# Optimization experiments

Hardware: AMD Instinct MI355X
Metric: run time of the kernel (lower is better)

## Reference

```python
import jax, jax.numpy as jnp
import numpy as np

IN_CH = 128
OUT_CH = 32
HEADS = 4
N_NODES = 50000
N_EDGES = 500000
NEG_SLOPE = 0.01  # torch leaky_relu default


def setup_inputs() -> dict:
    key = jax.random.key(0)
    ks = jax.random.split(key, 8)
    E, D, H, C = N_EDGES, IN_CH, HEADS, OUT_CH
    receivers = jax.random.normal(ks[0], (E, D), dtype=jnp.float32)
    senders = jax.random.normal(ks[1], (E, D), dtype=jnp.float32)
    edge_attribute = jax.random.normal(ks[2], (E, D), dtype=jnp.float32)
    sender_idx = jax.random.randint(ks[3], (E,), 0, N_NODES)
    receiver_idx = jax.random.randint(ks[4], (E,), 0, N_NODES)
    # bias-free linear weights, stored as [in, heads*out] so y = x @ W
    scale = 1.0 / np.sqrt(D)
    W_src = jax.random.normal(ks[5], (D, H * C), dtype=jnp.float32) * scale
    W_tgt = jax.random.normal(ks[6], (D, H * C), dtype=jnp.float32) * scale
    W_edge = jax.random.normal(ks[7], (D, H * C), dtype=jnp.float32) * scale
    # xavier_normal_ on shape (1, H, C): std = sqrt(2/(H + C)) per torch fan calc on last two dims
    attn = jax.random.normal(jax.random.fold_in(key, 99), (1, H, C), dtype=jnp.float32) * np.sqrt(2.0 / (H + C))
    return {
        "receivers": receivers,
        "senders": senders,
        "edge_attribute": edge_attribute,
        "sender_idx": sender_idx,
        "receiver_idx": receiver_idx,
        "W_src": W_src,
        "W_tgt": W_tgt,
        "W_edge": W_edge,
        "attn": attn,
    }


def reference(receivers, senders, edge_attribute, sender_idx, receiver_idx, W_src, W_tgt, W_edge, attn):
    E = receivers.shape[0]
    H, C = HEADS, OUT_CH
    t = (receivers @ W_tgt).reshape(E, H, C)   # target projection of receiver feats
    s = (senders @ W_src).reshape(E, H, C)
    e = (edge_attribute @ W_edge).reshape(E, H, C)
    z = (jax.nn.leaky_relu(s + t + e, NEG_SLOPE) * attn).sum(-1)  # [E, H]
    # segment softmax over edges grouped by sender_idx
    zmax = jax.ops.segment_max(z, sender_idx, num_segments=N_NODES)  # [N, H]
    ez = jnp.exp(z - zmax[sender_idx])
    denom = jax.ops.segment_sum(ez, sender_idx, num_segments=N_NODES)
    a = ez / denom[sender_idx]                 # [E, H]
    m = t * a[..., None]                        # [E, H, C]
    aggr_m = jax.ops.segment_sum(m, receiver_idx, num_segments=N_NODES)  # [N, H, C]
    return aggr_m.mean(axis=1), m.mean(axis=1)  # ([N, C], [E, C])
```

## Files before the change

kernel.cpp:

```cpp
#include <hip/hip_runtime.h>
#include <hip/hip_bf16.h>

#define E_EDGES 500000
#define NN 50000

typedef unsigned short u16;
typedef __attribute__((ext_vector_type(8))) short s16x8;
typedef __attribute__((ext_vector_type(4))) float f32x4;

#define BAR() __builtin_amdgcn_s_barrier()
#define SCHED0() __builtin_amdgcn_sched_barrier(0)
#define WAITLGKM0() asm volatile("s_waitcnt lgkmcnt(0)" ::: "memory")

__device__ __forceinline__ short f2bf(float f) {
    unsigned u = __builtin_bit_cast(unsigned, f);
    u += 0x7fffu + ((u >> 16) & 1u);
    return (short)(u >> 16);
}

__device__ __forceinline__ float lrelu(float x) { return x > 0.0f ? x : 0.01f * x; }

__device__ __forceinline__ s16x8 cvt8(float4 lo, float4 hi) {
    union { s16x8 v; __hip_bfloat162 h[4]; } u;
    u.h[0] = __float22bfloat162_rn(make_float2(lo.x, lo.y));
    u.h[1] = __float22bfloat162_rn(make_float2(lo.z, lo.w));
    u.h[2] = __float22bfloat162_rn(make_float2(hi.x, hi.y));
    u.h[3] = __float22bfloat162_rn(make_float2(hi.z, hi.w));
    return u.v;
}

__global__ void kprep(const float* __restrict__ Wsrc, const float* __restrict__ Wtgt,
                      const float* __restrict__ Wedge, u16* __restrict__ WT) {
    int i = blockIdx.x * 256 + threadIdx.x;
    if (i >= 3 * 16384) return;
    int g = i >> 14, nk = i & 16383, n = nk >> 7, k = nk & 127;
    const float* W = (g == 0) ? Wsrc : (g == 1) ? Wtgt : Wedge;
    WT[i] = (u16)f2bf(W[k * 128 + n]);
}

__global__ __launch_bounds__(256, 2) void k1(
    const float* __restrict__ recv, const float* __restrict__ send,
    const float* __restrict__ eattr, const int* __restrict__ sidx,
    const u16* __restrict__ WT, const float* __restrict__ attn,
    float* __restrict__ ez, float* __restrict__ denom)
{
    __shared__ u16 ldsA[64][136];
    __shared__ float smEz[64][4];
    const int tid = threadIdx.x;
    const int lane = tid & 63, wv = tid >> 6;
    const int l15 = lane & 15, lg = (lane >> 4) & 3;
    const int b = blockIdx.x;

    const float* Xg[3] = {send, eattr, recv};
    const int bgoff[3] = {0, 2 * 16384, 1 * 16384};

    s16x8 bfr[3][4][2];
#pragma unroll
    for (int g = 0; g < 3; ++g)
#pragma unroll
        for (int kk = 0; kk < 4; ++kk)
#pragma unroll
            for (int nn = 0; nn < 2; ++nn)
                bfr[g][kk][nn] = *(const s16x8*)(WT + bgoff[g] +
                    ((wv * 2 + nn) * 16 + l15) * 128 + kk * 32 + lg * 8);

    const float av0 = attn[(wv * 2 + 0) * 16 + l15];
    const float av1 = attn[(wv * 2 + 1) * 16 + l15];

    f32x4 acc[4][2];
    float4 ra[4][2];

    auto issueA = [&](const float* X, int tileRow) {
#pragma unroll
        for (int q = 0; q < 4; ++q) {
            int idx = tid + 256 * q;
            int row = idx >> 4, gcol = (idx & 15) * 8;
            int ge = min(tileRow + row, E_EDGES - 1);
            const float* p = X + (size_t)ge * 128 + gcol;
            ra[q][0] = *(const float4*)p;
            ra[q][1] = *(const float4*)(p + 4);
        }
    };

    auto commitA = [&]() {
#pragma unroll
        for (int q = 0; q < 4; ++q) {
            int idx = tid + 256 * q;
            *(s16x8*)&ldsA[idx >> 4][(idx & 15) * 8] = cvt8(ra[q][0], ra[q][1]);
        }
    };

    auto mfma_ph = [&](const s16x8 (&bf)[4][2]) {
#pragma unroll
        for (int kk = 0; kk < 4; ++kk) {
            int k0 = kk * 32 + lg * 8;
#pragma unroll
            for (int m = 0; m < 4; ++m) {
                s16x8 a = *(const s16x8*)&ldsA[m * 16 + l15][k0];
                acc[m][0] = __builtin_amdgcn_mfma_f32_16x16x32_bf16(a, bf[kk][0], acc[m][0], 0, 0, 0);
                acc[m][1] = __builtin_amdgcn_mfma_f32_16x16x32_bf16(a, bf[kk][1], acc[m][1], 0, 0, 0);
            }
        }
    };

    const int nt = (b < 645) ? 8 : 7;
    issueA(Xg[0], b * 64);

    for (int i = 0; i < nt; ++i) {
        const int tile = b + i * 1024;
        const int row0 = tile * 64;

#pragma unroll
        for (int m = 0; m < 4; ++m)
#pragma unroll
            for (int nn = 0; nn < 2; ++nn) acc[m][nn] = (f32x4){0.f, 0.f, 0.f, 0.f};

#pragma unroll
        for (int g = 0; g < 3; ++g) {
            if (g == 1) { mfma_ph(bfr[0]); SCHED0(); }
            if (g == 2) { mfma_ph(bfr[1]); SCHED0(); }
            BAR();
            commitA();
            if (g < 2) issueA(Xg[g + 1], row0);
            else if (i + 1 < nt) issueA(Xg[0], row0 + 65536);
            SCHED0();
            WAITLGKM0();
            BAR();
        }
        mfma_ph(bfr[2]);

#pragma unroll
        for (int m = 0; m < 4; ++m) {
            float part[4];
#pragma unroll
            for (int j = 0; j < 4; ++j)
                part[j] = lrelu(acc[m][0][j]) * av0 + lrelu(acc[m][1][j]) * av1;
#pragma unroll
            for (int off = 1; off < 16; off <<= 1) {
#pragma unroll
                for (int j = 0; j < 4; ++j) part[j] += __shfl_xor(part[j], off, 64);
            }
            if (l15 == 0) {
#pragma unroll
                for (int j = 0; j < 4; ++j)
                    smEz[m * 16 + lg * 4 + j][wv] = __expf(part[j]);
            }
        }
        __syncthreads();
        {
            int row = tid >> 2, h = tid & 3;
            int r = row0 + row;
            float v = smEz[row][h];
            if (r < E_EDGES) {
                ez[(size_t)r * 4 + h] = v;
                int s = sidx[r];
                atomicAdd(&denom[(size_t)s * 4 + h], v);
            }
        }
    }
}

__global__ __launch_bounds__(256, 2) void k2(
    const float* __restrict__ recv, const int* __restrict__ ridx,
    const int* __restrict__ sidx, const u16* __restrict__ WTt,
    const float* __restrict__ ez, const float* __restrict__ denom,
    float* __restrict__ out0, float* __restrict__ out1)
{
    __shared__ u16 ldsA[64][136];
    __shared__ u16 ldsB[128][136];
    const int tid = threadIdx.x;
    const int lane = tid & 63, wv = tid >> 6;
    const int l15 = lane & 15, lg = (lane >> 4) & 3;
    const int row0 = blockIdx.x * 64;

    float4 ra[4][2];
#pragma unroll
    for (int q = 0; q < 4; ++q) {
        int idx = tid + 256 * q;
        int row = idx >> 4, gcol = (idx & 15) * 8;
        int ge = min(row0 + row, E_EDGES - 1);
        const float* p = recv + (size_t)ge * 128 + gcol;
        ra[q][0] = *(const float4*)p;
        ra[q][1] = *(const float4*)(p + 4);
    }
    s16x8 rb[8];
#pragma unroll
    for (int q = 0; q < 8; ++q) {
        int idx = tid + 256 * q;
        rb[q] = *(const s16x8*)(WTt + (idx >> 4) * 128 + (idx & 15) * 8);
    }
#pragma unroll
    for (int q = 0; q < 4; ++q) {
        int idx = tid + 256 * q;
        *(s16x8*)&ldsA[idx >> 4][(idx & 15) * 8] = cvt8(ra[q][0], ra[q][1]);
    }
#pragma unroll
    for (int q = 0; q < 8; ++q) {
        int idx = tid + 256 * q;
        *(s16x8*)&ldsB[idx >> 4][(idx & 15) * 8] = rb[q];
    }
    __syncthreads();

    f32x4 acc[8];
#pragma unroll
    for (int n = 0; n < 8; ++n) acc[n] = (f32x4){0.f, 0.f, 0.f, 0.f};

#pragma unroll
    for (int kk = 0; kk < 4; ++kk) {
        int k0 = kk * 32 + lg * 8;
        s16x8 a = *(const s16x8*)&ldsA[wv * 16 + l15][k0];
#pragma unroll
        for (int n = 0; n < 8; ++n) {
            s16x8 b = *(const s16x8*)&ldsB[n * 16 + l15][k0];
            acc[n] = __builtin_amdgcn_mfma_f32_16x16x32_bf16(a, b, acc[n], 0, 0, 0);
        }
    }

#pragma unroll
    for (int j = 0; j < 4; ++j) {
        int r = row0 + wv * 16 + lg * 4 + j;
        if (r < E_EDGES) {
            int s = sidx[r];
            float4 ezv = *(const float4*)(ez + (size_t)r * 4);
            float4 dn = *(const float4*)(denom + (size_t)s * 4);
            float a0 = ezv.x / dn.x, a1 = ezv.y / dn.y;
            float a2 = ezv.z / dn.z, a3 = ezv.w / dn.w;
            float lo = 0.25f * (acc[0][j] * a0 + acc[2][j] * a1 +
                                acc[4][j] * a2 + acc[6][j] * a3);
            float hi = 0.25f * (acc[1][j] * a0 + acc[3][j] * a1 +
                                acc[5][j] * a2 + acc[7][j] * a3);
            out1[(size_t)r * 32 + l15] = lo;
            out1[(size_t)r * 32 + 16 + l15] = hi;
            int rv = ridx[r];
            atomicAdd(&out0[(size_t)rv * 32 + l15], lo);
            atomicAdd(&out0[(size_t)rv * 32 + 16 + l15], hi);
        }
    }
}

extern "C" void kernel_launch(void* const* d_in, const int* in_sizes, int n_in,
                              void* d_out, int out_size, void* d_ws, size_t ws_size,
                              hipStream_t stream) {
    const float* recv  = (const float*)d_in[0];
    const float* send  = (const float*)d_in[1];
    const float* eattr = (const float*)d_in[2];
    const int*   sidx  = (const int*)d_in[3];
    const int*   ridx  = (const int*)d_in[4];
    const float* Wsrc  = (const float*)d_in[5];
    const float* Wtgt  = (const float*)d_in[6];
    const float* Wedge = (const float*)d_in[7];
    const float* attn  = (const float*)d_in[8];

    char* ws = (char*)d_ws;
    u16*   WT    = (u16*)ws;
    float* ez    = (float*)(ws + 131072);
    float* denom = (float*)(ws + 131072 + 8000000);

    float* out0 = (float*)d_out;
    float* out1 = out0 + (size_t)NN * 32;

    hipMemsetAsync(denom, 0, (size_t)NN * 4 * sizeof(float), stream);
    hipMemsetAsync(out0, 0, (size_t)NN * 32 * sizeof(float), stream);

    kprep<<<192, 256, 0, stream>>>(Wsrc, Wtgt, Wedge, WT);

    k1<<<1024, 256, 0, stream>>>(recv, send, eattr, sidx, WT, attn, ez, denom);
    int nb2 = (E_EDGES + 63) / 64;
    k2<<<nb2, 256, 0, stream>>>(recv, ridx, sidx, WT + 16384, ez, denom, out0, out1);
}
```

Baseline: 276.3 us.

## Replace persistent pipelined k1 with one-tile-per-block grid loading all three inputs

k1 no longer loops persistently over 7-8 tiles per block with a software pipeline that overlapped each matrix's global load with the previous matrix's MFMA. Each block now handles a single 64-row tile. It loads all three input matrices at once into registers (12 float4 pairs per thread), converts them to bf16 into a tripled LDS buffer, and runs the three GEMM phases back to back. The grid grows from 1024 to about 7813 blocks, so latency hiding comes from more resident waves instead of explicit prefetch. The cost is higher register and LDS use (about 52KB per block), which may lower occupancy.

Result: slower. 307.0 us (+11.1%).

```diff
diff --git a/kernel.cpp b/kernel.cpp
--- a/kernel.cpp
+++ b/kernel.cpp
@@ -44,12 +44,11 @@
     const u16* __restrict__ WT, const float* __restrict__ attn,
     float* __restrict__ ez, float* __restrict__ denom)
 {
-    __shared__ u16 ldsA[64][136];
+    __shared__ u16 ldsA[3][64][136];
     __shared__ float smEz[64][4];
     const int tid = threadIdx.x;
     const int lane = tid & 63, wv = tid >> 6;
     const int l15 = lane & 15, lg = (lane >> 4) & 3;
-    const int b = blockIdx.x;
 
     const float* Xg[3] = {send, eattr, recv};
     const int bgoff[3] = {0, 2 * 16384, 1 * 16384};
@@ -68,15 +67,16 @@
     const float av1 = attn[(wv * 2 + 1) * 16 + l15];
 
     f32x4 acc[4][2];
-    float4 ra[4][2];
-
-    auto issueA = [&](const float* X, int tileRow) {
-#pragma unroll
-        for (int q = 0; q < 4; ++q) {
+    float4 ra[12][2];
+
+    auto issueA = [&](int tileRow) {
+#pragma unroll
+        for (int q = 0; q < 12; ++q) {
             int idx = tid + 256 * q;
-            int row = idx >> 4, gcol = (idx & 15) * 8;
+            int mat = idx >> 10, rem = idx & 1023;
+            int row = rem >> 4, gcol = (rem & 15) * 8;
             int ge = min(tileRow + row, E_EDGES - 1);
-            const float* p = X + (size_t)ge * 128 + gcol;
+            const float* p = Xg[mat] + (size_t)ge * 128 + gcol;
             ra[q][0] = *(const float4*)p;
             ra[q][1] = *(const float4*)(p + 4);
         }
@@ -84,78 +84,67 @@
 
     auto commitA = [&]() {
 #pragma unroll
-        for (int q = 0; q < 4; ++q) {
+        for (int q = 0; q < 12; ++q) {
             int idx = tid + 256 * q;
-            *(s16x8*)&ldsA[idx >> 4][(idx & 15) * 8] = cvt8(ra[q][0], ra[q][1]);
+            int mat = idx >> 10, rem = idx & 1023;
+            *(s16x8*)&ldsA[mat][rem >> 4][(rem & 15) * 8] = cvt8(ra[q][0], ra[q][1]);
         }
     };
 
-    auto mfma_ph = [&](const s16x8 (&bf)[4][2]) {
+    const int b = blockIdx.x;
+    const int row0 = b * 64;
+
+    issueA(row0);
+    SCHED0();
+    commitA();
+    WAITLGKM0();
+    BAR();
+
+#pragma unroll
+    for (int m = 0; m < 4; ++m)
+#pragma unroll
+        for (int nn = 0; nn < 2; ++nn) acc[m][nn] = (f32x4){0.f, 0.f, 0.f, 0.f};
+
+#pragma unroll
+    for (int g = 0; g < 3; ++g) {
 #pragma unroll
         for (int kk = 0; kk < 4; ++kk) {
             int k0 = kk * 32 + lg * 8;
 #pragma unroll
             for (int m = 0; m < 4; ++m) {
-                s16x8 a = *(const s16x8*)&ldsA[m * 16 + l15][k0];
-                acc[m][0] = __builtin_amdgcn_mfma_f32_16x16x32_bf16(a, bf[kk][0], acc[m][0], 0, 0, 0);
-                acc[m][1] = __builtin_amdgcn_mfma_f32_16x16x32_bf16(a, bf[kk][1], acc[m][1], 0, 0, 0);
+                s16x8 a = *(const s16x8*)&ldsA[g][m * 16 + l15][k0];
+                acc[m][0] = __builtin_amdgcn_mfma_f32_16x16x32_bf16(a, bfr[g][kk][0], acc[m][0], 0, 0, 0);
+                acc[m][1] = __builtin_amdgcn_mfma_f32_16x16x32_bf16(a, bfr[g][kk][1], acc[m][1], 0, 0, 0);
             }
         }
-    };
-
-    const int nt = (b < 645) ? 8 : 7;
-    issueA(Xg[0], b * 64);
-
-    for (int i = 0; i < nt; ++i) {
-        const int tile = b + i * 1024;
-        const int row0 = tile * 64;
-
-#pragma unroll
-        for (int m = 0; m < 4; ++m)
-#pragma unroll
-            for (int nn = 0; nn < 2; ++nn) acc[m][nn] = (f32x4){0.f, 0.f, 0.f, 0.f};
-
-#pragma unroll
-        for (int g = 0; g < 3; ++g) {
-            if (g == 1) { mfma_ph(bfr[0]); SCHED0(); }
-            if (g == 2) { mfma_ph(bfr[1]); SCHED0(); }
-            BAR();
-            commitA();
-            if (g < 2) issueA(Xg[g + 1], row0);
-            else if (i + 1 < nt) issueA(Xg[0], row0 + 65536);
-            SCHED0();
-            WAITLGKM0();
-            BAR();
-        }
-        mfma_ph(bfr[2]);
-
-#pragma unroll
-        for (int m = 0; m < 4; ++m) {
-            float part[4];
+    }
+
+#pragma unroll
+    for (int m = 0; m < 4; ++m) {
+        float part[4];
+#pragma unroll
+        for (int j = 0; j < 4; ++j)
+            part[j] = lrelu(acc[m][0][j]) * av0 + lrelu(acc[m][1][j]) * av1;
+#pragma unroll
+        for (int off = 1; off < 16; off <<= 1) {
+#pragma unroll
+            for (int j = 0; j < 4; ++j) part[j] += __shfl_xor(part[j], off, 64);
+        }
+        if (l15 == 0) {
 #pragma unroll
             for (int j = 0; j < 4; ++j)
-                part[j] = lrelu(acc[m][0][j]) * av0 + lrelu(acc[m][1][j]) * av1;
-#pragma unroll
-            for (int off = 1; off < 16; off <<= 1) {
-#pragma unroll
-                for (int j = 0; j < 4; ++j) part[j] += __shfl_xor(part[j], off, 64);
-            }
-            if (l15 == 0) {
-#pragma unroll
-                for (int j = 0; j < 4; ++j)
-                    smEz[m * 16 + lg * 4 + j][wv] = __expf(part[j]);
-            }
-        }
-        __syncthreads();
-        {
-            int row = tid >> 2, h = tid & 3;
-            int r = row0 + row;
-            float v = smEz[row][h];
-            if (r < E_EDGES) {
-                ez[(size_t)r * 4 + h] = v;
-                int s = sidx[r];
-                atomicAdd(&denom[(size_t)s * 4 + h], v);
-            }
+                smEz[m * 16 + lg * 4 + j][wv] = __expf(part[j]);
+        }
+    }
+    __syncthreads();
+    {
+        int row = tid >> 2, h = tid & 3;
+        int r = row0 + row;
+        float v = smEz[row][h];
+        if (r < E_EDGES) {
+            ez[(size_t)r * 4 + h] = v;
+            int s = sidx[r];
+            atomicAdd(&denom[(size_t)s * 4 + h], v);
         }
     }
 }
@@ -264,7 +253,7 @@
 
     kprep<<<192, 256, 0, stream>>>(Wsrc, Wtgt, Wedge, WT);
 
-    k1<<<1024, 256, 0, stream>>>(recv, send, eattr, sidx, WT, attn, ez, denom);
-    int nb2 = (E_EDGES + 63) / 64;
-    k2<<<nb2, 256, 0, stream>>>(recv, ridx, sidx, WT + 16384, ez, denom, out0, out1);
-}
+    int nb = (E_EDGES + 63) / 64;
+    k1<<<nb, 256, 0, stream>>>(recv, send, eattr, sidx, WT, attn, ez, denom);
+    k2<<<nb, 256, 0, stream>>>(recv, ridx, sidx, WT + 16384, ez, denom, out0, out1);
+}
```
